# Performance work log

Measured on AMD Instinct MI355X. Metric: run time of the kernel, lower is better.

The kernel has to match this reference:

```python
import jax, jax.numpy as jnp
import numpy as np

EMBED_DIM = 512
NUM_HEADS = 8
HEAD_DIM = EMBED_DIM // NUM_HEADS
REL_MAX = 16
NUM_POS_IDS = 2 * REL_MAX + 1 + 1  # 34 (directed + padding id)
PADDING_IDX = 0
B, S = 2, 2048


def setup_inputs() -> dict:
    key = jax.random.key(0)
    ks = jax.random.split(key, 9)
    Q = jax.random.normal(ks[0], (B, S, EMBED_DIM), dtype=jnp.float32)
    K = jax.random.normal(ks[1], (B, S, EMBED_DIM), dtype=jnp.float32)
    V = jax.random.normal(ks[2], (B, S, EMBED_DIM), dtype=jnp.float32)
    rel_pos_ids = jax.random.randint(ks[3], (B, S, S), 0, NUM_POS_IDS, dtype=jnp.int64) if jax.config.jax_enable_x64 else jax.random.randint(ks[3], (B, S, S), 0, NUM_POS_IDS, dtype=jnp.int32)
    scale = 0.02
    Wq = jax.random.normal(ks[4], (EMBED_DIM, EMBED_DIM), dtype=jnp.float32) * scale
    Wk = jax.random.normal(ks[5], (EMBED_DIM, EMBED_DIM), dtype=jnp.float32) * scale
    Wv = jax.random.normal(ks[6], (EMBED_DIM, EMBED_DIM), dtype=jnp.float32) * scale
    Wo = jax.random.normal(ks[7], (EMBED_DIM, EMBED_DIM), dtype=jnp.float32) * scale
    rel_emb = jax.random.normal(ks[8], (NUM_POS_IDS, EMBED_DIM), dtype=jnp.float32) * scale
    rel_emb = rel_emb.at[PADDING_IDX].set(0.0)  # nn.Embedding padding_idx row is zero
    return {"Q": Q, "K": K, "V": V, "rel_pos_ids": rel_pos_ids,
            "Wq": Wq, "Wk": Wk, "Wv": Wv, "Wo": Wo, "rel_emb": rel_emb}


def _proj(x, W):
    # Linear (no bias) then strided head split: view(B, S, head_dim, H) -> (B, H, S, head_dim)
    b, s, _ = x.shape
    y = x @ W.T
    return y.reshape(b, s, HEAD_DIM, NUM_HEADS).transpose(0, 3, 1, 2)


def _forward(Q, K, V, rel_pos_ids, Wq, Wk, Wv, Wo, rel_emb):
    b, sq, _ = Q.shape
    Qp = _proj(Q, Wq)  # (B, H, Sq, hd)
    Kp = _proj(K, Wk)  # (B, H, Sk, hd)
    Vp = _proj(V, Wv)  # (B, H, Sk, hd)

    # rel_embeds split per head with the same strided layout: (P, hd, H) -> (H, P, hd)
    R = rel_emb.reshape(NUM_POS_IDS, HEAD_DIM, NUM_HEADS).transpose(2, 0, 1)
    # Q_rel: (B, H, Sq, P)
    Q_rel = jnp.einsum('bhsd,hpd->bhsp', Qp, R)
    # gather per-pair relative bias: (B, H, Sq, Sk)
    rel_shift = jnp.take_along_axis(Q_rel, rel_pos_ids[:, None, :, :], axis=3)
    mask = (rel_pos_ids == PADDING_IDX)[:, None, :, :]
    rel_shift = jnp.where(mask, -jnp.inf, rel_shift)

    energy = (jnp.einsum('bhqd,bhkd->bhqk', Qp, Kp) + rel_shift) / jnp.sqrt(jnp.float32(HEAD_DIM))
    attn = jax.nn.softmax(energy, axis=-1)
    out = jnp.einsum('bhqk,bhkd->bhqd', attn, Vp)  # (B, H, Sq, hd)
    # inverse of strided split: (B, Sq, hd, H) -> flatten last two
    out = out.transpose(0, 2, 3, 1).reshape(b, sq, EMBED_DIM)
    return out @ Wo.T


def reference(Q, K, V, rel_pos_ids, Wq, Wk, Wv, Wo, rel_emb):
    return _forward(Q, K, V, rel_pos_ids, Wq, Wk, Wv, Wo, rel_emb)
```

## Files before the change

### kernel.cpp

```cpp
#include <hip/hip_runtime.h>
#include <cstdint>
#include <cstddef>

#define SEQ   2048
#define BBAT  2
#define EMBED 512
#define NH    8
#define HD    64
#define NPOS  34

typedef __bf16 bf16;
typedef __bf16 bf16x8 __attribute__((ext_vector_type(8)));
typedef float  f32x4  __attribute__((ext_vector_type(4)));
typedef int    int32x4 __attribute__((ext_vector_type(4)));

#define ESCALE 0.1803368801111204f

__device__ __forceinline__ f32x4 mfma16(bf16x8 a, bf16x8 b, f32x4 c){
  return __builtin_amdgcn_mfma_f32_16x16x32_bf16(a, b, c, 0, 0, 0);
}

__device__ __forceinline__ void barrier_lgkm(){
  asm volatile("s_waitcnt lgkmcnt(0)" ::: "memory");
  __builtin_amdgcn_s_barrier();
  __builtin_amdgcn_sched_barrier(0);
}

__global__ __launch_bounds__(256) void k_prep(
    const float* __restrict__ Q, const float* __restrict__ K, const float* __restrict__ V,
    const float* __restrict__ Wq, const float* __restrict__ Wk,
    const float* __restrict__ Wv, const float* __restrict__ Wo,
    const float* __restrict__ RE,
    bf16* __restrict__ Qb, bf16* __restrict__ Kb, bf16* __restrict__ Vb,
    bf16* __restrict__ Wall, bf16* __restrict__ Rb)
{
  const int NCONV = 3*524288;
  const int NW = 196608, NO = 262144;
  int i = blockIdx.x*256 + threadIdx.x;
  if (i < NCONV){
    int tsel = i >> 19, j = i & 524287;
    const float* s = tsel==0 ? Q : (tsel==1 ? K : V);
    bf16* d       = tsel==0 ? Qb : (tsel==1 ? Kb : Vb);
    float4 v = ((const float4*)s)[j];
    union { bf16 e[4]; ushort4 u; } pk;
    pk.e[0]=(bf16)v.x; pk.e[1]=(bf16)v.y; pk.e[2]=(bf16)v.z; pk.e[3]=(bf16)v.w;
    ((ushort4*)d)[j] = pk.u;
  } else {
    int j = i - NCONV;
    if (j < NW){
      int w  = j >> 16;
      int r  = j & 65535;
      int np = r >> 7, c4 = (r & 127) << 2;
      const float* W = (w==0) ? Wq : ((w==1) ? Wk : Wv);
      int src = ((np & 63) << 3) + (np >> 6);
      float4 v = *(const float4*)(W + (size_t)src*512 + c4);
      union { bf16 e[4]; ushort4 u; } pk;
      pk.e[0]=(bf16)v.x; pk.e[1]=(bf16)v.y; pk.e[2]=(bf16)v.z; pk.e[3]=(bf16)v.w;
      *(ushort4*)(Wall + (size_t)w*262144 + (size_t)np*512 + c4) = pk.u;
    } else if (j < NW + NO){
      int jj = j - NW;
      int n = jj >> 9, kp = jj & 511;
      int src = ((kp & 63) << 3) + (kp >> 6);
      Wall[(size_t)3*262144 + (size_t)n*512 + kp] = (bf16)Wo[(size_t)n*512 + src];
    } else {
      int jj = j - NW - NO;
      if (jj < 8*48*64){
        int h  = jj / (48*64);
        int r2 = jj - h*(48*64);
        int p  = r2 >> 6, dd = r2 & 63;
        float v = (p < NPOS) ? RE[(size_t)p*512 + dd*8 + h] : 0.f;
        Rb[jj] = (bf16)v;
      }
    }
  }
}

__global__ __launch_bounds__(256,2) void k_proj(
    const bf16* __restrict__ Qb, const bf16* __restrict__ Kb, const bf16* __restrict__ Vb,
    const bf16* __restrict__ W,
    bf16* __restrict__ Qp, bf16* __restrict__ Kp, bf16* __restrict__ Vt)
{
  const int z = blockIdx.z;
  const bf16* A  = z==0 ? Qb : (z==1 ? Kb : Vb);
  const bf16* Bw = W + (size_t)z*262144;

  __shared__ __align__(16) bf16 AB[2][128][72];
  bf16 (*As)[72] = AB[0];
  bf16 (*Bs)[72] = AB[1];

  const int t = threadIdx.x;
  const int w = t >> 6, lane = t & 63, l15 = lane & 15, quad = lane >> 4;
  const int wm = (w & 1) * 64, wn = (w >> 1) * 64;
  const int m0 = blockIdx.y * 128, n0 = blockIdx.x * 128;
  const int row = t >> 3, c8 = (t & 7) << 3;

  const bf16* Abase = A  + (size_t)(m0 + row)*512 + c8;
  const bf16* Bbase = Bw + (size_t)(n0 + row)*512 + c8;

  uint4 pa0,pa1,pa2,pa3, pb0,pb1,pb2,pb3;
  uint4 qa0,qa1,qa2,qa3, qb0,qb1,qb2,qb3;
  pa0 = *(const uint4*)(Abase);
  pa1 = *(const uint4*)(Abase + 32*512);
  pa2 = *(const uint4*)(Abase + 64*512);
  pa3 = *(const uint4*)(Abase + 96*512);
  pb0 = *(const uint4*)(Bbase);
  pb1 = *(const uint4*)(Bbase + 32*512);
  pb2 = *(const uint4*)(Bbase + 64*512);
  pb3 = *(const uint4*)(Bbase + 96*512);

  f32x4 acc[4][4];
  #pragma unroll
  for (int mt=0; mt<4; ++mt)
    #pragma unroll
    for (int nt=0; nt<4; ++nt) acc[mt][nt] = (f32x4){0.f,0.f,0.f,0.f};

#define PROJ_BODY(KT, A0,A1,A2,A3, B0,B1,B2,B3, LA0,LA1,LA2,LA3, LB0,LB1,LB2,LB3) \
  {                                                                             \
    barrier_lgkm();                       \
    *(uint4*)&As[row     ][c8] = A0;                                            \
    *(uint4*)&As[row + 32][c8] = A1;                                            \
    *(uint4*)&As[row + 64][c8] = A2;                                            \
    *(uint4*)&As[row + 96][c8] = A3;                                            \
    *(uint4*)&Bs[row     ][c8] = B0;                                            \
    *(uint4*)&Bs[row + 32][c8] = B1;                                            \
    *(uint4*)&Bs[row + 64][c8] = B2;                                            \
    *(uint4*)&Bs[row + 96][c8] = B3;                                            \
    if ((KT) < 7){                                                              \
      const bf16* ap2 = Abase + ((KT)+1)*64;                                    \
      const bf16* bp2 = Bbase + ((KT)+1)*64;                                    \
      LA0 = *(const uint4*)(ap2);                                               \
      LA1 = *(const uint4*)(ap2 + 32*512);                                      \
      LA2 = *(const uint4*)(ap2 + 64*512);                                      \
      LA3 = *(const uint4*)(ap2 + 96*512);                                      \
      LB0 = *(const uint4*)(bp2);                                               \
      LB1 = *(const uint4*)(bp2 + 32*512);                                      \
      LB2 = *(const uint4*)(bp2 + 64*512);                                      \
      LB3 = *(const uint4*)(bp2 + 96*512);                                      \
    }                                                                           \
    barrier_lgkm();                  \
    __builtin_amdgcn_s_setprio(1);                                              \
    _Pragma("unroll")                                                           \
    for (int ks = 0; ks < 2; ++ks){                                             \
      bf16x8 am[4], bn[4];                                                      \
      _Pragma("unroll")                                                         \
      for (int x=0;x<4;++x) am[x] = *(const bf16x8*)&As[wm + x*16 + l15][ks*32 + quad*8]; \
      _Pragma("unroll")                                                         \
      for (int y=0;y<4;++y) bn[y] = *(const bf16x8*)&Bs[wn + y*16 + l15][ks*32 + quad*8]; \
      _Pragma("unroll")                                                         \
      for (int mt=0;mt<4;++mt)                                                  \
        _Pragma("unroll")                                                       \
        for (int nt=0;nt<4;++nt)                                                \
          acc[mt][nt] = mfma16(am[mt], bn[nt], acc[mt][nt]);                    \
    }                                                                           \
    __builtin_amdgcn_s_setprio(0);                                              \
  }

  for (int kt2 = 0; kt2 < 8; kt2 += 2){
    PROJ_BODY(kt2,     pa0,pa1,pa2,pa3, pb0,pb1,pb2,pb3, qa0,qa1,qa2,qa3, qb0,qb1,qb2,qb3)
    PROJ_BODY(kt2 + 1, qa0,qa1,qa2,qa3, qb0,qb1,qb2,qb3, pa0,pa1,pa2,pa3, pb0,pb1,pb2,pb3)
  }
#undef PROJ_BODY

  if (z != 2){
    bf16* C = z==0 ? Qp : Kp;
    const float scl = (z==0) ? ESCALE : 1.0f;
    #pragma unroll
    for (int mt=0;mt<4;++mt)
      #pragma unroll
      for (int r=0;r<4;++r){
        int m = m0 + wm + mt*16 + quad*4 + r;
        #pragma unroll
        for (int nt=0;nt<4;++nt)
          C[(size_t)m*512 + n0 + wn + nt*16 + l15] = (bf16)(acc[mt][nt][r] * scl);
      }
  } else {
    __syncthreads();
    bf16 (*VT)[136] = (bf16(*)[136])AB;
    #pragma unroll
    for (int mt=0;mt<4;++mt)
      #pragma unroll
      for (int r=0;r<4;++r){
        int m = wm + mt*16 + quad*4 + r;
        #pragma unroll
        for (int nt=0;nt<4;++nt)
          VT[wn + nt*16 + l15][m] = (bf16)acc[mt][nt][r];
      }
    __syncthreads();
    const int b = m0 >> 11, s0 = m0 & 2047;
    const int n = t >> 1, c0 = (t & 1) * 64;
    const int h = blockIdx.x*2 + (n >> 6), d = n & 63;
    bf16* dst = Vt + ((size_t)((b*NH + h)*HD + d))*SEQ + s0 + c0;
    #pragma unroll
    for (int i = 0; i < 8; ++i)
      *(uint4*)(dst + i*8) = *(const uint4*)&VT[n][c0 + i*8];
  }
}

__global__ __launch_bounds__(256,2) void k_gemm_out(
    const bf16* __restrict__ A, const bf16* __restrict__ Bw, float* __restrict__ C)
{
  __shared__ __align__(16) bf16 AB[2][128][72];
  bf16 (*As)[72] = AB[0];
  bf16 (*Bs)[72] = AB[1];

  const int t = threadIdx.x;
  const int w = t >> 6, lane = t & 63, l15 = lane & 15, quad = lane >> 4;
  const int wm = (w & 1) * 64, wn = (w >> 1) * 64;
  const int m0 = blockIdx.y * 128, n0 = blockIdx.x * 128;
  const int row = t >> 3, c8 = (t & 7) << 3;

  const bf16* Abase = A  + (size_t)(m0 + row)*512 + c8;
  const bf16* Bbase = Bw + (size_t)(n0 + row)*512 + c8;

  uint4 pa0,pa1,pa2,pa3, pb0,pb1,pb2,pb3;
  uint4 qa0,qa1,qa2,qa3, qb0,qb1,qb2,qb3;
  pa0 = *(const uint4*)(Abase);
  pa1 = *(const uint4*)(Abase + 32*512);
  pa2 = *(const uint4*)(Abase + 64*512);
  pa3 = *(const uint4*)(Abase + 96*512);
  pb0 = *(const uint4*)(Bbase);
  pb1 = *(const uint4*)(Bbase + 32*512);
  pb2 = *(const uint4*)(Bbase + 64*512);
  pb3 = *(const uint4*)(Bbase + 96*512);

  f32x4 acc[4][4];
  #pragma unroll
  for (int mt=0; mt<4; ++mt)
    #pragma unroll
    for (int nt=0; nt<4; ++nt) acc[mt][nt] = (f32x4){0.f,0.f,0.f,0.f};

#define OUT_BODY(KT, A0,A1,A2,A3, B0,B1,B2,B3, LA0,LA1,LA2,LA3, LB0,LB1,LB2,LB3) \
  {                                                                             \
    barrier_lgkm();                                                             \
    *(uint4*)&As[row     ][c8] = A0;                                            \
    *(uint4*)&As[row + 32][c8] = A1;                                            \
    *(uint4*)&As[row + 64][c8] = A2;                                            \
    *(uint4*)&As[row + 96][c8] = A3;                                            \
    *(uint4*)&Bs[row     ][c8] = B0;                                            \
    *(uint4*)&Bs[row + 32][c8] = B1;                                            \
    *(uint4*)&Bs[row + 64][c8] = B2;                                            \
    *(uint4*)&Bs[row + 96][c8] = B3;                                            \
    if ((KT) < 7){                                                              \
      const bf16* ap2 = Abase + ((KT)+1)*64;                                    \
      const bf16* bp2 = Bbase + ((KT)+1)*64;                                    \
      LA0 = *(const uint4*)(ap2);                                               \
      LA1 = *(const uint4*)(ap2 + 32*512);                                      \
      LA2 = *(const uint4*)(ap2 + 64*512);                                      \
      LA3 = *(const uint4*)(ap2 + 96*512);                                      \
      LB0 = *(const uint4*)(bp2);                                               \
      LB1 = *(const uint4*)(bp2 + 32*512);                                      \
      LB2 = *(const uint4*)(bp2 + 64*512);                                      \
      LB3 = *(const uint4*)(bp2 + 96*512);                                      \
    }                                                                           \
    barrier_lgkm();                                                             \
    __builtin_amdgcn_s_setprio(1);                                              \
    _Pragma("unroll")                                                           \
    for (int ks = 0; ks < 2; ++ks){                                             \
      bf16x8 am[4], bn[4];                                                      \
      _Pragma("unroll")                                                         \
      for (int x=0;x<4;++x) am[x] = *(const bf16x8*)&As[wm + x*16 + l15][ks*32 + quad*8]; \
      _Pragma("unroll")                                                         \
      for (int y=0;y<4;++y) bn[y] = *(const bf16x8*)&Bs[wn + y*16 + l15][ks*32 + quad*8]; \
      _Pragma("unroll")                                                         \
      for (int mt=0;mt<4;++mt)                                                  \
        _Pragma("unroll")                                                       \
        for (int nt=0;nt<4;++nt)                                                \
          acc[mt][nt] = mfma16(am[mt], bn[nt], acc[mt][nt]);                    \
    }                                                                           \
    __builtin_amdgcn_s_setprio(0);                                              \
  }

  for (int kt2 = 0; kt2 < 8; kt2 += 2){
    OUT_BODY(kt2,     pa0,pa1,pa2,pa3, pb0,pb1,pb2,pb3, qa0,qa1,qa2,qa3, qb0,qb1,qb2,qb3)
    OUT_BODY(kt2 + 1, qa0,qa1,qa2,qa3, qb0,qb1,qb2,qb3, pa0,pa1,pa2,pa3, pb0,pb1,pb2,pb3)
  }
#undef OUT_BODY

  #pragma unroll
  for (int mt=0;mt<4;++mt)
    #pragma unroll
    for (int r=0;r<4;++r){
      int m = m0 + wm + mt*16 + quad*4 + r;
      #pragma unroll
      for (int nt=0;nt<4;++nt)
        C[(size_t)m*512 + n0 + wn + nt*16 + l15] = acc[mt][nt][r];
    }
}

__global__ __launch_bounds__(256,2) void k_attn(
    const bf16* __restrict__ Qp, const bf16* __restrict__ Kp,
    const bf16* __restrict__ Vt, const bf16* __restrict__ Rb,
    const int* __restrict__ ids, bf16* __restrict__ Out)
{
  __shared__ __align__(16) bf16 Ks[128][72];
  __shared__ __align__(16) bf16 Vs[64][136];
  __shared__ __align__(16) bf16 Ps[64][136];
  __shared__ float lutT[35][65];
  __shared__ float lsum_s[128];

  const int t = threadIdx.x;
  const int b = blockIdx.z, h = blockIdx.y;
  const int q0 = blockIdx.x * 64;
  const int w = t >> 6, lane = t & 63, l15 = lane & 15, quad = lane >> 4;
  const int qh = w & 1, kh = w >> 1;

  const size_t idb = (size_t)b*SEQ*SEQ;
  const bf16* kbase = Kp + (size_t)b*SEQ*EMBED + h*HD;
  const bf16* vbase = Vt + (size_t)(b*NH + h)*HD*SEQ;

  const int krow = t >> 3, kcol = (t & 7) << 3;
  const int vrow = t >> 4, vcol = (t & 15) << 3;

  uint4 ka0, ka1, ka2, ka3, va0, va1, va2, va3;
  uint4 kb0, kb1, kb2, kb3, vb0, vb1, vb2, vb3;
  ka0 = *(const uint4*)(kbase + (size_t)(krow     )*EMBED + kcol);
  ka1 = *(const uint4*)(kbase + (size_t)(krow + 32)*EMBED + kcol);
  ka2 = *(const uint4*)(kbase + (size_t)(krow + 64)*EMBED + kcol);
  ka3 = *(const uint4*)(kbase + (size_t)(krow + 96)*EMBED + kcol);
  va0 = *(const uint4*)(vbase + (size_t)(vrow     )*SEQ + vcol);
  va1 = *(const uint4*)(vbase + (size_t)(vrow + 16)*SEQ + vcol);
  va2 = *(const uint4*)(vbase + (size_t)(vrow + 32)*SEQ + vcol);
  va3 = *(const uint4*)(vbase + (size_t)(vrow + 48)*SEQ + vcol);

  int32x4 nid[2][4];
  #pragma unroll
  for (int mt=0; mt<2; ++mt)
    #pragma unroll
    for (int nt=0; nt<4; ++nt)
      nid[mt][nt] = *(const int32x4*)(ids + idb
          + (size_t)(q0 + qh*32 + mt*16 + l15)*SEQ
          + kh*64 + nt*16 + quad*4);

  {
    const bf16* qbrow = Qp + (size_t)(b*SEQ + q0 + w*16 + l15)*EMBED + h*HD;
    bf16x8 ab0 = *(const bf16x8*)(qbrow + quad*8);
    bf16x8 ab1 = *(const bf16x8*)(qbrow + 32 + quad*8);
    const bf16* rh = Rb + h*3072;
    #pragma unroll
    for (int nt = 0; nt < 3; ++nt){
      bf16x8 r0 = *(const bf16x8*)(rh + (nt*16 + l15)*64 + quad*8);
      bf16x8 r1 = *(const bf16x8*)(rh + (nt*16 + l15)*64 + 32 + quad*8);
      f32x4 c = (f32x4){0.f,0.f,0.f,0.f};
      c = mfma16(ab0, r0, c);
      c = mfma16(ab1, r1, c);
      int p = nt*16 + l15;
      if (p < NPOS){
        #pragma unroll
        for (int r = 0; r < 4; ++r)
          lutT[p][w*16 + quad*4 + r] = (p == 0) ? -1e30f : c[r];
      }
    }
  }

  bf16x8 bq[2][2];
  #pragma unroll
  for (int mt = 0; mt < 2; ++mt){
    const bf16* qrow = Qp + (size_t)(b*SEQ + q0 + qh*32 + mt*16 + l15)*EMBED + h*HD;
    bq[mt][0] = *(const bf16x8*)(qrow + quad*8);
    bq[mt][1] = *(const bf16x8*)(qrow + 32 + quad*8);
  }

  f32x4 acc[2][4];
  #pragma unroll
  for (int mt=0;mt<2;++mt)
    #pragma unroll
    for (int nt=0;nt<4;++nt) acc[mt][nt] = (f32x4){0.f,0.f,0.f,0.f};
  float lsum[2] = {0.f, 0.f};

#define ATTN_BODY(KT, K0,K1,K2,K3, V0,V1,V2,V3, L0,L1,L2,L3, M0,M1,M2,M3)       \
  {                                                                             \
    barrier_lgkm();              \
    *(uint4*)&Ks[krow     ][kcol] = K0;                                         \
    *(uint4*)&Ks[krow + 32][kcol] = K1;                                         \
    *(uint4*)&Ks[krow + 64][kcol] = K2;                                         \
    *(uint4*)&Ks[krow + 96][kcol] = K3;                                         \
    *(uint4*)&Vs[vrow     ][vcol] = V0;                                         \
    *(uint4*)&Vs[vrow + 16][vcol] = V1;                                         \
    *(uint4*)&Vs[vrow + 32][vcol] = V2;                                         \
    *(uint4*)&Vs[vrow + 48][vcol] = V3;                                         \
    if ((KT) < 15){                                                             \
      const bf16* kp2 = kbase + (size_t)(((KT)+1)*128)*EMBED + kcol;            \
      const bf16* vp2 = vbase + ((KT)+1)*128 + vcol;                            \
      L0 = *(const uint4*)(kp2 + (size_t)(krow     )*EMBED);                    \
      L1 = *(const uint4*)(kp2 + (size_t)(krow + 32)*EMBED);                    \
      L2 = *(const uint4*)(kp2 + (size_t)(krow + 64)*EMBED);                    \
      L3 = *(const uint4*)(kp2 + (size_t)(krow + 96)*EMBED);                    \
      M0 = *(const uint4*)(vp2 + (size_t)(vrow     )*SEQ);                      \
      M1 = *(const uint4*)(vp2 + (size_t)(vrow + 16)*SEQ);                      \
      M2 = *(const uint4*)(vp2 + (size_t)(vrow + 32)*SEQ);                      \
      M3 = *(const uint4*)(vp2 + (size_t)(vrow + 48)*SEQ);                      \
    }                                                                           \
    barrier_lgkm();                \
    float wvv[2][4][4];                                                         \
    _Pragma("unroll")                                                           \
    for (int mt = 0; mt < 2; ++mt){                                             \
      const float* lcol = &lutT[0][qh*32 + mt*16 + l15];                        \
      _Pragma("unroll")                                                         \
      for (int nt = 0; nt < 4; ++nt){                                           \
        int32x4 v = nid[mt][nt];                                                \
        wvv[mt][nt][0] = lcol[v[0] * 65];                                       \
        wvv[mt][nt][1] = lcol[v[1] * 65];                                       \
        wvv[mt][nt][2] = lcol[v[2] * 65];                                       \
        wvv[mt][nt][3] = lcol[v[3] * 65];                                       \
      }                                                                         \
    }                                                                           \
    if ((KT) < 15){                                                             \
      _Pragma("unroll")                                                         \
      for (int mt = 0; mt < 2; ++mt)                                            \
        _Pragma("unroll")                                                       \
        for (int nt = 0; nt < 4; ++nt)                                          \
          nid[mt][nt] = *(const int32x4*)(ids + idb                             \
              + (size_t)(q0 + qh*32 + mt*16 + l15)*SEQ                          \
              + (((KT)+1)*128) + kh*64 + nt*16 + quad*4);                       \
    }                                                                           \
    f32x4 sf[2][4];                                                             \
    __builtin_amdgcn_s_setprio(1);                                              \
    _Pragma("unroll")                                                           \
    for (int nt = 0; nt < 4; ++nt){                                             \
      bf16x8 ak0 = *(const bf16x8*)&Ks[kh*64 + nt*16 + l15][quad*8];            \
      bf16x8 ak1 = *(const bf16x8*)&Ks[kh*64 + nt*16 + l15][32 + quad*8];       \
      _Pragma("unroll")                                                         \
      for (int mt = 0; mt < 2; ++mt){                                           \
        f32x4 c = (f32x4){0.f,0.f,0.f,0.f};                                     \
        c = mfma16(ak0, bq[mt][0], c);                                          \
        c = mfma16(ak1, bq[mt][1], c);                                          \
        sf[mt][nt] = c;                                                         \
      }                                                                         \
    }                                                                           \
    __builtin_amdgcn_s_setprio(0);                                              \
    _Pragma("unroll")                                                           \
    for (int mt = 0; mt < 2; ++mt){                                             \
      _Pragma("unroll")                                                         \
      for (int nt = 0; nt < 4; ++nt){                                           \
        union { bf16 e[4]; uint2 u; } pk;                                       \
        float p0 = __builtin_amdgcn_exp2f(sf[mt][nt][0] + wvv[mt][nt][0]);      \
        float p1 = __builtin_amdgcn_exp2f(sf[mt][nt][1] + wvv[mt][nt][1]);      \
        float p2 = __builtin_amdgcn_exp2f(sf[mt][nt][2] + wvv[mt][nt][2]);      \
        float p3 = __builtin_amdgcn_exp2f(sf[mt][nt][3] + wvv[mt][nt][3]);      \
        pk.e[0] = (bf16)p0; pk.e[1] = (bf16)p1;                                 \
        pk.e[2] = (bf16)p2; pk.e[3] = (bf16)p3;                                 \
        lsum[mt] += (p0 + p1) + (p2 + p3);                                      \
        *(uint2*)&Ps[qh*32 + mt*16 + l15][kh*64 + nt*16 + quad*4] = pk.u;       \
      }                                                                         \
    }                                                                           \
    __builtin_amdgcn_s_setprio(1);                                              \
    _Pragma("unroll")                                                           \
    for (int ks = 0; ks < 2; ++ks){                                             \
      bf16x8 ap[2];                                                             \
      _Pragma("unroll")                                                         \
      for (int mt = 0; mt < 2; ++mt)                                            \
        ap[mt] = *(const bf16x8*)&Ps[qh*32 + mt*16 + l15][kh*64 + ks*32 + quad*8]; \
      _Pragma("unroll")                                                         \
      for (int nt = 0; nt < 4; ++nt){                                           \
        bf16x8 bv = *(const bf16x8*)&Vs[nt*16 + l15][kh*64 + ks*32 + quad*8];   \
        _Pragma("unroll")                                                       \
        for (int mt = 0; mt < 2; ++mt)                                          \
          acc[mt][nt] = mfma16(ap[mt], bv, acc[mt][nt]);                        \
      }                                                                         \
    }                                                                           \
    __builtin_amdgcn_s_setprio(0);                                              \
  }

  for (int kt2 = 0; kt2 < 16; kt2 += 2){
    ATTN_BODY(kt2,     ka0,ka1,ka2,ka3, va0,va1,va2,va3, kb0,kb1,kb2,kb3, vb0,vb1,vb2,vb3)
    ATTN_BODY(kt2 + 1, kb0,kb1,kb2,kb3, vb0,vb1,vb2,vb3, ka0,ka1,ka2,ka3, va0,va1,va2,va3)
  }
#undef ATTN_BODY

  __syncthreads();

  #pragma unroll
  for (int mt = 0; mt < 2; ++mt){
    float v = lsum[mt];
    v += __shfl_xor(v, 16);
    v += __shfl_xor(v, 32);
    if (quad == 0) lsum_s[kh*64 + qh*32 + mt*16 + l15] = v;
  }

  float* xch = (float*)&Ps[0][0];
  if (kh == 1){
    #pragma unroll
    for (int mt = 0; mt < 2; ++mt)
      #pragma unroll
      for (int nt = 0; nt < 4; ++nt){
        f32x4 a = acc[mt][nt];
        #pragma unroll
        for (int r = 0; r < 4; ++r)
          xch[(qh*32 + mt*16 + quad*4 + r)*65 + nt*16 + l15] = a[r];
      }
  }
  __syncthreads();

  if (kh == 0){
    #pragma unroll
    for (int mt = 0; mt < 2; ++mt){
      #pragma unroll
      for (int r = 0; r < 4; ++r){
        int ql = qh*32 + mt*16 + quad*4 + r;
        float inv = __builtin_amdgcn_rcpf(lsum_s[ql] + lsum_s[64 + ql]);
        #pragma unroll
        for (int nt = 0; nt < 4; ++nt){
          float o = acc[mt][nt][r] + xch[ql*65 + nt*16 + l15];
          Out[(size_t)(b*SEQ + q0 + ql)*EMBED + h*HD + nt*16 + l15] = (bf16)(o*inv);
        }
      }
    }
  }
}

extern "C" void kernel_launch(void* const* d_in, const int* in_sizes, int n_in,
                              void* d_out, int out_size, void* d_ws, size_t ws_size,
                              hipStream_t stream)
{
  (void)in_sizes; (void)n_in; (void)out_size;
  const float* Q  = (const float*)d_in[0];
  const float* K  = (const float*)d_in[1];
  const float* V  = (const float*)d_in[2];
  const int*   ID = (const int*)d_in[3];
  const float* Wq = (const float*)d_in[4];
  const float* Wk = (const float*)d_in[5];
  const float* Wv = (const float*)d_in[6];
  const float* Wo = (const float*)d_in[7];
  const float* RE = (const float*)d_in[8];
  float* out = (float*)d_out;

  const size_t MB = (size_t)1 << 20;
  if (ws_size < 36*MB) return;
  char* ws = (char*)d_ws;
  bf16*  Qb    = (bf16*)(ws + 0*MB);
  bf16*  Kb    = (bf16*)(ws + 4*MB);
  bf16*  Vb    = (bf16*)(ws + 8*MB);
  bf16*  Qp    = (bf16*)(ws + 12*MB);
  bf16*  Kp    = (bf16*)(ws + 16*MB);
  bf16*  Vt    = (bf16*)(ws + 20*MB);
  bf16*  Wall  = (bf16*)(ws + 24*MB);
  bf16*  Wop   = Wall + (size_t)3*262144;
  bf16*  Rb    = (bf16*)(ws + 26*MB);
  bf16*  AO    = (bf16*)(ws + 0*MB);

  k_prep      <<<dim3(8032),    256, 0, stream>>>(Q, K, V, Wq, Wk, Wv, Wo, RE,
                                                  Qb, Kb, Vb, Wall, Rb);
  k_proj      <<<dim3(4,32,3),  256, 0, stream>>>(Qb, Kb, Vb, Wall, Qp, Kp, Vt);
  k_attn      <<<dim3(32,8,2),  256, 0, stream>>>(Qp, Kp, Vt, Rb, ID, AO);
  k_gemm_out  <<<dim3(4,32),    256, 0, stream>>>(AO, Wop, out);
}
```

Before: 179.6 us.

## Load K/V MFMA fragments directly from global memory, dropping LDS staging and barriers

The attention kernel no longer stages K and V tiles through shared memory. Each wave now loads its own MFMA operand fragments straight into registers: K is double-buffered and prefetched after the QK MFMAs, and V is prefetched after the PV MFMAs. Because every wave reads back only the P tile it wrote itself, the two per-tile block barriers go away. An XOR swizzle on the P tile in shared memory is added to reduce bank conflicts. The cost is duplicated global/L2 traffic, since waves sharing a key half fetch the same fragments, plus extra register pressure and less latency hiding for the single-buffered V loads.

```diff
diff --git a/kernel.cpp b/kernel.cpp
--- a/kernel.cpp
+++ b/kernel.cpp
@@ -18,6 +18,10 @@
 
 __device__ __forceinline__ f32x4 mfma16(bf16x8 a, bf16x8 b, f32x4 c){
   return __builtin_amdgcn_mfma_f32_16x16x32_bf16(a, b, c, 0, 0, 0);
+}
+
+__device__ __forceinline__ bf16x8 asbf(uint4 x){
+  union { uint4 u; bf16x8 v; } c; c.u = x; return c.v;
 }
 
 __device__ __forceinline__ void barrier_lgkm(){
@@ -116,7 +120,7 @@
 
 #define PROJ_BODY(KT, A0,A1,A2,A3, B0,B1,B2,B3, LA0,LA1,LA2,LA3, LB0,LB1,LB2,LB3) \
   {                                                                             \
-    barrier_lgkm();                       \
+    barrier_lgkm();                                                             \
     *(uint4*)&As[row     ][c8] = A0;                                            \
     *(uint4*)&As[row + 32][c8] = A1;                                            \
     *(uint4*)&As[row + 64][c8] = A2;                                            \
@@ -137,7 +141,7 @@
       LB2 = *(const uint4*)(bp2 + 64*512);                                      \
       LB3 = *(const uint4*)(bp2 + 96*512);                                      \
     }                                                                           \
-    barrier_lgkm();                  \
+    barrier_lgkm();                                                             \
     __builtin_amdgcn_s_setprio(1);                                              \
     _Pragma("unroll")                                                           \
     for (int ks = 0; ks < 2; ++ks){                                             \
@@ -292,8 +296,6 @@
     const bf16* __restrict__ Vt, const bf16* __restrict__ Rb,
     const int* __restrict__ ids, bf16* __restrict__ Out)
 {
-  __shared__ __align__(16) bf16 Ks[128][72];
-  __shared__ __align__(16) bf16 Vs[64][136];
   __shared__ __align__(16) bf16 Ps[64][136];
   __shared__ float lutT[35][65];
   __shared__ float lsum_s[128];
@@ -303,24 +305,42 @@
   const int q0 = blockIdx.x * 64;
   const int w = t >> 6, lane = t & 63, l15 = lane & 15, quad = lane >> 4;
   const int qh = w & 1, kh = w >> 1;
+  const int psw = l15 & 8;
 
   const size_t idb = (size_t)b*SEQ*SEQ;
-  const bf16* kbase = Kp + (size_t)b*SEQ*EMBED + h*HD;
-  const bf16* vbase = Vt + (size_t)(b*NH + h)*HD*SEQ;
-
-  const int krow = t >> 3, kcol = (t & 7) << 3;
-  const int vrow = t >> 4, vcol = (t & 15) << 3;
-
-  uint4 ka0, ka1, ka2, ka3, va0, va1, va2, va3;
-  uint4 kb0, kb1, kb2, kb3, vb0, vb1, vb2, vb3;
-  ka0 = *(const uint4*)(kbase + (size_t)(krow     )*EMBED + kcol);
-  ka1 = *(const uint4*)(kbase + (size_t)(krow + 32)*EMBED + kcol);
-  ka2 = *(const uint4*)(kbase + (size_t)(krow + 64)*EMBED + kcol);
-  ka3 = *(const uint4*)(kbase + (size_t)(krow + 96)*EMBED + kcol);
-  va0 = *(const uint4*)(vbase + (size_t)(vrow     )*SEQ + vcol);
-  va1 = *(const uint4*)(vbase + (size_t)(vrow + 16)*SEQ + vcol);
-  va2 = *(const uint4*)(vbase + (size_t)(vrow + 32)*SEQ + vcol);
-  va3 = *(const uint4*)(vbase + (size_t)(vrow + 48)*SEQ + vcol);
+  const bf16* kfr = Kp + (size_t)b*SEQ*EMBED + h*HD
+                  + (size_t)(kh*64 + l15)*EMBED + quad*8;
+  const bf16* vfr = Vt + (size_t)(b*NH + h)*HD*SEQ
+                  + (size_t)l15*SEQ + kh*64 + quad*8;
+
+  uint4 fk0,fk1,fk2,fk3,fk4,fk5,fk6,fk7;
+  uint4 gk0,gk1,gk2,gk3,gk4,gk5,gk6,gk7;
+  uint4 sv0,sv1,sv2,sv3,sv4,sv5,sv6,sv7;
+
+#define LOAD_K(KT, K0,K1,K2,K3,K4,K5,K6,K7)                                    \
+  { const bf16* kp2 = kfr + (size_t)(KT)*128*EMBED;                            \
+    K0 = *(const uint4*)(kp2);                                                 \
+    K1 = *(const uint4*)(kp2 + 32);                                            \
+    K2 = *(const uint4*)(kp2 + 16*EMBED);                                      \
+    K3 = *(const uint4*)(kp2 + 16*EMBED + 32);                                 \
+    K4 = *(const uint4*)(kp2 + 32*EMBED);                                      \
+    K5 = *(const uint4*)(kp2 + 32*EMBED + 32);                                 \
+    K6 = *(const uint4*)(kp2 + 48*EMBED);                                      \
+    K7 = *(const uint4*)(kp2 + 48*EMBED + 32); }
+
+#define LOAD_V(KT)                                                             \
+  { const bf16* vp2 = vfr + (KT)*128;                                          \
+    sv0 = *(const uint4*)(vp2);                                                \
+    sv1 = *(const uint4*)(vp2 + 32);                                           \
+    sv2 = *(const uint4*)(vp2 + 16*SEQ);                                       \
+    sv3 = *(const uint4*)(vp2 + 16*SEQ + 32);                                  \
+    sv4 = *(const uint4*)(vp2 + 32*SEQ);                                       \
+    sv5 = *(const uint4*)(vp2 + 32*SEQ + 32);                                  \
+    sv6 = *(const uint4*)(vp2 + 48*SEQ);                                       \
+    sv7 = *(const uint4*)(vp2 + 48*SEQ + 32); }
+
+  LOAD_K(0, fk0,fk1,fk2,fk3,fk4,fk5,fk6,fk7)
+  LOAD_V(0)
 
   int32x4 nid[2][4];
   #pragma unroll
@@ -360,6 +380,8 @@
     bq[mt][1] = *(const bf16x8*)(qrow + 32 + quad*8);
   }
 
+  __syncthreads();
+
   f32x4 acc[2][4];
   #pragma unroll
   for (int mt=0;mt<2;++mt)
@@ -367,105 +389,104 @@
     for (int nt=0;nt<4;++nt) acc[mt][nt] = (f32x4){0.f,0.f,0.f,0.f};
   float lsum[2] = {0.f, 0.f};
 
-#define ATTN_BODY(KT, K0,K1,K2,K3, V0,V1,V2,V3, L0,L1,L2,L3, M0,M1,M2,M3)       \
-  {                                                                             \
-    barrier_lgkm();              \
-    *(uint4*)&Ks[krow     ][kcol] = K0;                                         \
-    *(uint4*)&Ks[krow + 32][kcol] = K1;                                         \
-    *(uint4*)&Ks[krow + 64][kcol] = K2;                                         \
-    *(uint4*)&Ks[krow + 96][kcol] = K3;                                         \
-    *(uint4*)&Vs[vrow     ][vcol] = V0;                                         \
-    *(uint4*)&Vs[vrow + 16][vcol] = V1;                                         \
-    *(uint4*)&Vs[vrow + 32][vcol] = V2;                                         \
-    *(uint4*)&Vs[vrow + 48][vcol] = V3;                                         \
-    if ((KT) < 15){                                                             \
-      const bf16* kp2 = kbase + (size_t)(((KT)+1)*128)*EMBED + kcol;            \
-      const bf16* vp2 = vbase + ((KT)+1)*128 + vcol;                            \
-      L0 = *(const uint4*)(kp2 + (size_t)(krow     )*EMBED);                    \
-      L1 = *(const uint4*)(kp2 + (size_t)(krow + 32)*EMBED);                    \
-      L2 = *(const uint4*)(kp2 + (size_t)(krow + 64)*EMBED);                    \
-      L3 = *(const uint4*)(kp2 + (size_t)(krow + 96)*EMBED);                    \
-      M0 = *(const uint4*)(vp2 + (size_t)(vrow     )*SEQ);                      \
-      M1 = *(const uint4*)(vp2 + (size_t)(vrow + 16)*SEQ);                      \
-      M2 = *(const uint4*)(vp2 + (size_t)(vrow + 32)*SEQ);                      \
-      M3 = *(const uint4*)(vp2 + (size_t)(vrow + 48)*SEQ);                      \
-    }                                                                           \
-    barrier_lgkm();                \
-    float wvv[2][4][4];                                                         \
-    _Pragma("unroll")                                                           \
-    for (int mt = 0; mt < 2; ++mt){                                             \
-      const float* lcol = &lutT[0][qh*32 + mt*16 + l15];                        \
-      _Pragma("unroll")                                                         \
-      for (int nt = 0; nt < 4; ++nt){                                           \
-        int32x4 v = nid[mt][nt];                                                \
-        wvv[mt][nt][0] = lcol[v[0] * 65];                                       \
-        wvv[mt][nt][1] = lcol[v[1] * 65];                                       \
-        wvv[mt][nt][2] = lcol[v[2] * 65];                                       \
-        wvv[mt][nt][3] = lcol[v[3] * 65];                                       \
-      }                                                                         \
-    }                                                                           \
-    if ((KT) < 15){                                                             \
-      _Pragma("unroll")                                                         \
-      for (int mt = 0; mt < 2; ++mt)                                            \
-        _Pragma("unroll")                                                       \
-        for (int nt = 0; nt < 4; ++nt)                                          \
-          nid[mt][nt] = *(const int32x4*)(ids + idb                             \
-              + (size_t)(q0 + qh*32 + mt*16 + l15)*SEQ                          \
-              + (((KT)+1)*128) + kh*64 + nt*16 + quad*4);                       \
-    }                                                                           \
-    f32x4 sf[2][4];                                                             \
-    __builtin_amdgcn_s_setprio(1);                                              \
-    _Pragma("unroll")                                                           \
-    for (int nt = 0; nt < 4; ++nt){                                             \
-      bf16x8 ak0 = *(const bf16x8*)&Ks[kh*64 + nt*16 + l15][quad*8];            \
-      bf16x8 ak1 = *(const bf16x8*)&Ks[kh*64 + nt*16 + l15][32 + quad*8];       \
-      _Pragma("unroll")                                                         \
-      for (int mt = 0; mt < 2; ++mt){                                           \
-        f32x4 c = (f32x4){0.f,0.f,0.f,0.f};                                     \
-        c = mfma16(ak0, bq[mt][0], c);                                          \
-        c = mfma16(ak1, bq[mt][1], c);                                          \
-        sf[mt][nt] = c;                                                         \
-      }                                                                         \
-    }                                                                           \
-    __builtin_amdgcn_s_setprio(0);                                              \
-    _Pragma("unroll")                                                           \
-    for (int mt = 0; mt < 2; ++mt){                                             \
-      _Pragma("unroll")                                                         \
-      for (int nt = 0; nt < 4; ++nt){                                           \
-        union { bf16 e[4]; uint2 u; } pk;                                       \
-        float p0 = __builtin_amdgcn_exp2f(sf[mt][nt][0] + wvv[mt][nt][0]);      \
-        float p1 = __builtin_amdgcn_exp2f(sf[mt][nt][1] + wvv[mt][nt][1]);      \
-        float p2 = __builtin_amdgcn_exp2f(sf[mt][nt][2] + wvv[mt][nt][2]);      \
-        float p3 = __builtin_amdgcn_exp2f(sf[mt][nt][3] + wvv[mt][nt][3]);      \
-        pk.e[0] = (bf16)p0; pk.e[1] = (bf16)p1;                                 \
-        pk.e[2] = (bf16)p2; pk.e[3] = (bf16)p3;                                 \
-        lsum[mt] += (p0 + p1) + (p2 + p3);                                      \
-        *(uint2*)&Ps[qh*32 + mt*16 + l15][kh*64 + nt*16 + quad*4] = pk.u;       \
-      }                                                                         \
-    }                                                                           \
-    __builtin_amdgcn_s_setprio(1);                                              \
-    _Pragma("unroll")                                                           \
-    for (int ks = 0; ks < 2; ++ks){                                             \
-      bf16x8 ap[2];                                                             \
-      _Pragma("unroll")                                                         \
-      for (int mt = 0; mt < 2; ++mt)                                            \
-        ap[mt] = *(const bf16x8*)&Ps[qh*32 + mt*16 + l15][kh*64 + ks*32 + quad*8]; \
-      _Pragma("unroll")                                                         \
-      for (int nt = 0; nt < 4; ++nt){                                           \
-        bf16x8 bv = *(const bf16x8*)&Vs[nt*16 + l15][kh*64 + ks*32 + quad*8];   \
-        _Pragma("unroll")                                                       \
-        for (int mt = 0; mt < 2; ++mt)                                          \
-          acc[mt][nt] = mfma16(ap[mt], bv, acc[mt][nt]);                        \
-      }                                                                         \
-    }                                                                           \
-    __builtin_amdgcn_s_setprio(0);                                              \
+#define ATTN_TILE(KT, K0,K1,K2,K3,K4,K5,K6,K7, L0,L1,L2,L3,L4,L5,L6,L7)        \
+  {                                                                            \
+    float wvv[2][4][4];                                                        \
+    _Pragma("unroll")                                                          \
+    for (int mt = 0; mt < 2; ++mt){                                            \
+      const float* lcol = &lutT[0][qh*32 + mt*16 + l15];                       \
+      _Pragma("unroll")                                                        \
+      for (int nt = 0; nt < 4; ++nt){                                          \
+        int32x4 v = nid[mt][nt];                                               \
+        wvv[mt][nt][0] = lcol[v[0] * 65];                                      \
+        wvv[mt][nt][1] = lcol[v[1] * 65];                                      \
+        wvv[mt][nt][2] = lcol[v[2] * 65];                                      \
+        wvv[mt][nt][3] = lcol[v[3] * 65];                                      \
+      }                                                                        \
+    }                                                                          \
+    if ((KT) < 15){                                                            \
+      _Pragma("unroll")                                                        \
+      for (int mt = 0; mt < 2; ++mt)                                           \
+        _Pragma("unroll")                                                      \
+        for (int nt = 0; nt < 4; ++nt)                                         \
+          nid[mt][nt] = *(const int32x4*)(ids + idb                            \
+              + (size_t)(q0 + qh*32 + mt*16 + l15)*SEQ                         \
+              + (((KT)+1)*128) + kh*64 + nt*16 + quad*4);                      \
+    }                                                                          \
+    f32x4 sf[2][4];                                                            \
+    __builtin_amdgcn_s_setprio(1);                                             \
+    {                                                                          \
+      f32x4 c;                                                                 \
+      c = (f32x4){0.f,0.f,0.f,0.f};                                            \
+      c = mfma16(asbf(K0), bq[0][0], c); sf[0][0] = mfma16(asbf(K1), bq[0][1], c); \
+      c = (f32x4){0.f,0.f,0.f,0.f};                                            \
+      c = mfma16(asbf(K0), bq[1][0], c); sf[1][0] = mfma16(asbf(K1), bq[1][1], c); \
+      c = (f32x4){0.f,0.f,0.f,0.f};                                            \
+      c = mfma16(asbf(K2), bq[0][0], c); sf[0][1] = mfma16(asbf(K3), bq[0][1], c); \
+      c = (f32x4){0.f,0.f,0.f,0.f};                                            \
+      c = mfma16(asbf(K2), bq[1][0], c); sf[1][1] = mfma16(asbf(K3), bq[1][1], c); \
+      c = (f32x4){0.f,0.f,0.f,0.f};                                            \
+      c = mfma16(asbf(K4), bq[0][0], c); sf[0][2] = mfma16(asbf(K5), bq[0][1], c); \
+      c = (f32x4){0.f,0.f,0.f,0.f};                                            \
+      c = mfma16(asbf(K4), bq[1][0], c); sf[1][2] = mfma16(asbf(K5), bq[1][1], c); \
+      c = (f32x4){0.f,0.f,0.f,0.f};                                            \
+      c = mfma16(asbf(K6), bq[0][0], c); sf[0][3] = mfma16(asbf(K7), bq[0][1], c); \
+      c = (f32x4){0.f,0.f,0.f,0.f};                                            \
+      c = mfma16(asbf(K6), bq[1][0], c); sf[1][3] = mfma16(asbf(K7), bq[1][1], c); \
+    }                                                                          \
+    __builtin_amdgcn_s_setprio(0);                                             \
+    if ((KT) < 15){ LOAD_K((KT)+1, L0,L1,L2,L3,L4,L5,L6,L7) }                  \
+    _Pragma("unroll")                                                          \
+    for (int mt = 0; mt < 2; ++mt){                                            \
+      _Pragma("unroll")                                                        \
+      for (int nt = 0; nt < 4; ++nt){                                          \
+        union { bf16 e[4]; uint2 u; } pk;                                      \
+        float p0 = __builtin_amdgcn_exp2f(sf[mt][nt][0] + wvv[mt][nt][0]);     \
+        float p1 = __builtin_amdgcn_exp2f(sf[mt][nt][1] + wvv[mt][nt][1]);     \
+        float p2 = __builtin_amdgcn_exp2f(sf[mt][nt][2] + wvv[mt][nt][2]);     \
+        float p3 = __builtin_amdgcn_exp2f(sf[mt][nt][3] + wvv[mt][nt][3]);     \
+        pk.e[0] = (bf16)p0; pk.e[1] = (bf16)p1;                                \
+        pk.e[2] = (bf16)p2; pk.e[3] = (bf16)p3;                                \
+        lsum[mt] += (p0 + p1) + (p2 + p3);                                     \
+        *(uint2*)&Ps[qh*32 + mt*16 + l15]                                      \
+                    [(kh*64 + nt*16 + quad*4) ^ psw] = pk.u;                   \
+      }                                                                        \
+    }                                                                          \
+    __builtin_amdgcn_s_setprio(1);                                             \
+    {                                                                          \
+      bf16x8 ap0, ap1;                                                         \
+      ap0 = *(const bf16x8*)&Ps[qh*32 + l15][(kh*64 + quad*8) ^ psw];          \
+      ap1 = *(const bf16x8*)&Ps[qh*32 + 16 + l15][(kh*64 + quad*8) ^ psw];     \
+      acc[0][0] = mfma16(ap0, asbf(sv0), acc[0][0]);                           \
+      acc[1][0] = mfma16(ap1, asbf(sv0), acc[1][0]);                           \
+      acc[0][1] = mfma16(ap0, asbf(sv2), acc[0][1]);                           \
+      acc[1][1] = mfma16(ap1, asbf(sv2), acc[1][1]);                           \
+      acc[0][2] = mfma16(ap0, asbf(sv4), acc[0][2]);                           \
+      acc[1][2] = mfma16(ap1, asbf(sv4), acc[1][2]);                           \
+      acc[0][3] = mfma16(ap0, asbf(sv6), acc[0][3]);                           \
+      acc[1][3] = mfma16(ap1, asbf(sv6), acc[1][3]);                           \
+      ap0 = *(const bf16x8*)&Ps[qh*32 + l15][(kh*64 + 32 + quad*8) ^ psw];     \
+      ap1 = *(const bf16x8*)&Ps[qh*32 + 16 + l15][(kh*64 + 32 + quad*8) ^ psw];\
+      acc[0][0] = mfma16(ap0, asbf(sv1), acc[0][0]);                           \
+      acc[1][0] = mfma16(ap1, asbf(sv1), acc[1][0]);                           \
+      acc[0][1] = mfma16(ap0, asbf(sv3), acc[0][1]);                           \
+      acc[1][1] = mfma16(ap1, asbf(sv3), acc[1][1]);                           \
+      acc[0][2] = mfma16(ap0, asbf(sv5), acc[0][2]);                           \
+      acc[1][2] = mfma16(ap1, asbf(sv5), acc[1][2]);                           \
+      acc[0][3] = mfma16(ap0, asbf(sv7), acc[0][3]);                           \
+      acc[1][3] = mfma16(ap1, asbf(sv7), acc[1][3]);                           \
+    }                                                                          \
+    __builtin_amdgcn_s_setprio(0);                                             \
+    if ((KT) < 15){ LOAD_V((KT)+1) }                                           \
   }
 
   for (int kt2 = 0; kt2 < 16; kt2 += 2){
-    ATTN_BODY(kt2,     ka0,ka1,ka2,ka3, va0,va1,va2,va3, kb0,kb1,kb2,kb3, vb0,vb1,vb2,vb3)
-    ATTN_BODY(kt2 + 1, kb0,kb1,kb2,kb3, vb0,vb1,vb2,vb3, ka0,ka1,ka2,ka3, va0,va1,va2,va3)
-  }
-#undef ATTN_BODY
+    ATTN_TILE(kt2,     fk0,fk1,fk2,fk3,fk4,fk5,fk6,fk7, gk0,gk1,gk2,gk3,gk4,gk5,gk6,gk7)
+    ATTN_TILE(kt2 + 1, gk0,gk1,gk2,gk3,gk4,gk5,gk6,gk7, fk0,fk1,fk2,fk3,fk4,fk5,fk6,fk7)
+  }
+#undef ATTN_TILE
+#undef LOAD_K
+#undef LOAD_V
 
   __syncthreads();
 
```

Result: slower. 241.4 us (+34.4%).
